# Kernel optimization log

Hardware: AMD Instinct MI355X
Metric: run time of the kernel (lower is better)

## Reference

```python
import jax, jax.numpy as jnp
from jax import lax
import numpy as np

B, L, D_MODEL = 2, 2048, 1024
D_INNER, D_STATE, D_CONV, DT_RANK = 2048, 16, 4, 64


def setup_inputs() -> dict:
    key = jax.random.key(0)
    ks = jax.random.split(key, 10)
    s = 0.02  # weight scale to keep activations numerically sane
    return {
        "x": jax.random.normal(ks[0], (B, L, D_MODEL), jnp.float32),
        "W_in": jax.random.normal(ks[1], (D_MODEL, 2 * D_INNER), jnp.float32) * s,
        "conv_w": jax.random.normal(ks[2], (D_INNER, D_CONV), jnp.float32) * 0.2,
        "conv_b": jax.random.normal(ks[3], (D_INNER,), jnp.float32) * 0.1,
        "W_xproj": jax.random.normal(ks[4], (D_INNER, DT_RANK + 2 * D_STATE), jnp.float32) * s,
        "W_dt": jax.random.normal(ks[5], (DT_RANK, D_INNER), jnp.float32) * (DT_RANK ** -0.5),
        "b_dt": jax.random.normal(ks[6], (D_INNER,), jnp.float32) * 0.1,
        "A_log": jax.random.uniform(ks[7], (D_INNER, D_STATE), jnp.float32),
        "D_skip": jnp.ones((D_INNER,), jnp.float32),
        "W_out": jax.random.normal(ks[8], (D_INNER, D_MODEL), jnp.float32) * s,
    }


def _causal_depthwise_conv(xt, w, b):
    # xt: (B, L, d_inner), w: (d_inner, d_conv). Torch pads both sides by d_conv-1
    # then slices [:L] => causal left-pad of d_conv-1.
    xc = jnp.moveaxis(xt, 1, 2)  # (B, d_inner, L)
    out = lax.conv_general_dilated(
        xc, w[:, None, :], window_strides=(1,),
        padding=[(D_CONV - 1, 0)], feature_group_count=D_INNER)
    return jnp.moveaxis(out, 1, 2) + b  # (B, L, d_inner)


def _selective_scan(u, delta, A, Bm, Cm, D_skip):
    # u, delta: (B, L, d_inner); A: (d_inner, d_state); Bm, Cm: (B, L, d_state)
    deltaA = jnp.exp(delta[..., None] * A)                  # (B,L,di,ds)
    dBu = (delta * u)[..., None] * Bm[:, :, None, :]        # (B,L,di,ds)

    def step(h, inp):
        dA_t, dBu_t, C_t = inp                              # (B,di,ds),(B,di,ds),(B,ds)
        h = dA_t * h + dBu_t
        y = jnp.einsum('bds,bs->bd', h, C_t)
        return h, y

    h0 = jnp.zeros((u.shape[0], D_INNER, D_STATE), u.dtype)
    xs = (jnp.moveaxis(deltaA, 1, 0), jnp.moveaxis(dBu, 1, 0), jnp.moveaxis(Cm, 1, 0))
    _, ys = lax.scan(step, h0, xs)                          # ys: (L,B,di)
    return jnp.moveaxis(ys, 0, 1) + u * D_skip


def reference(x, W_in, conv_w, conv_b, W_xproj, W_dt, b_dt, A_log, D_skip, W_out):
    xz = x @ W_in                                           # (B,L,2*di)
    xin, z = jnp.split(xz, 2, axis=-1)
    xc = jax.nn.silu(_causal_depthwise_conv(xin, conv_w, conv_b))
    dbc = xc @ W_xproj                                      # (B,L,dt_rank+2*ds)
    dt_lo = dbc[..., :DT_RANK]
    Bm = dbc[..., DT_RANK:DT_RANK + D_STATE]
    Cm = dbc[..., DT_RANK + D_STATE:]
    delta = jax.nn.softplus(dt_lo @ W_dt + b_dt)            # (B,L,di)
    A = -jnp.exp(A_log)
    y = _selective_scan(xc, delta, A, Bm, Cm, D_skip)
    return (y * jax.nn.silu(z)) @ W_out                     # (B,L,d_model)
```

## Files before the change

### kernel.cpp

```cpp
#include <hip/hip_runtime.h>
#include <math.h>

#define B_SZ 2
#define L_SZ 2048
#define DMODEL 1024
#define DINNER 2048
#define DSTATE 16
#define DCONV 4
#define DTRANK 64

#define CS 32
#define NCH (L_SZ / CS)

typedef float f32x4 __attribute__((ext_vector_type(4)));
typedef __bf16 bf16x8 __attribute__((ext_vector_type(8)));

__device__ __forceinline__ float silu_f(float x) {
    return x / (1.0f + __expf(-x));
}

__device__ __forceinline__ float softplus_f(float x) {
    return fmaxf(x, 0.0f) + __logf(1.0f + __expf(-fabsf(x)));
}

__device__ __forceinline__ unsigned short f2bf(float x) {
    unsigned int u = __float_as_uint(x);
    u = u + 0x7FFFu + ((u >> 16) & 1u);
    return (unsigned short)(u >> 16);
}

__device__ __forceinline__ float bf2f(unsigned short s) {
    return __uint_as_float(((unsigned int)s) << 16);
}

__device__ __forceinline__ void gload_lds16(const unsigned short* g, unsigned short* l) {
    __builtin_amdgcn_global_load_lds(
        (const __attribute__((address_space(1))) void*)g,
        (__attribute__((address_space(3))) void*)l, 16, 0, 0);
}

union Pack8 { unsigned short s[8]; uint4 v; };

__global__ __launch_bounds__(256) void transpose_cast(
    const float* __restrict__ W, unsigned short* __restrict__ WT, int R, int C)
{
    __shared__ float t[32][33];
    const int tx = threadIdx.x & 31;
    const int ty = threadIdx.x >> 5;
    const int r0 = blockIdx.y * 32;
    const int c0 = blockIdx.x * 32;
    #pragma unroll
    for (int i = 0; i < 4; i++)
        t[ty + i * 8][tx] = W[(r0 + ty + i * 8) * C + c0 + tx];
    __syncthreads();
    #pragma unroll
    for (int i = 0; i < 4; i++)
        WT[(c0 + ty + i * 8) * R + r0 + tx] = f2bf(t[tx][ty + i * 8]);
}

__global__ __launch_bounds__(256) void cast_bf16(
    const float* __restrict__ src, unsigned short* __restrict__ dst, int n8)
{
    int i = blockIdx.x * 256 + threadIdx.x;
    if (i >= n8) return;
    const float4 f0 = *(const float4*)(src + i * 8);
    const float4 f1 = *(const float4*)(src + i * 8 + 4);
    Pack8 p;
    p.s[0] = f2bf(f0.x); p.s[1] = f2bf(f0.y); p.s[2] = f2bf(f0.z); p.s[3] = f2bf(f0.w);
    p.s[4] = f2bf(f1.x); p.s[5] = f2bf(f1.y); p.s[6] = f2bf(f1.z); p.s[7] = f2bf(f1.w);
    *(uint4*)(dst + i * 8) = p.v;
}

template <int ACT, int OBF16>
__global__ __launch_bounds__(256) void gemm_bt_lds(
    const unsigned short* __restrict__ A, const unsigned short* __restrict__ BT,
    void* __restrict__ Cout, const float* __restrict__ bias,
    int M, int N, int K, int lda, int ldb, int ldc, int Kc)
{
    __shared__ unsigned short As[128 * 64];
    __shared__ unsigned short Bs[128 * 64];

    const int tid  = threadIdx.x;
    const int lane = tid & 63;
    const int wave = tid >> 6;
    const int wm   = wave >> 1;
    const int wn   = wave & 1;
    const int row0 = blockIdx.y * 128;
    const int col0 = blockIdx.x * 128;
    const int lq   = lane >> 4;
    const int lm   = lane & 15;
    const int kbeg = blockIdx.z * Kc;

    const int rloc = wave * 32 + (lane >> 3);
    const int sc   = (lane & 7) ^ ((lane >> 3) & 7);
    const unsigned short* gA = A + (size_t)(row0 + rloc) * lda + sc * 8;
    const unsigned short* gBp[4];
    #pragma unroll
    for (int is = 0; is < 4; is++) {
        int br = col0 + rloc + 8 * is;
        if (br > N - 1) br = N - 1;
        gBp[is] = BT + (size_t)br * ldb + sc * 8;
    }
    unsigned short* lA = As + wave * 2048;
    unsigned short* lB = Bs + wave * 2048;

    f32x4 acc[4][4];
    #pragma unroll
    for (int i = 0; i < 4; i++)
        #pragma unroll
        for (int j = 0; j < 4; j++)
            #pragma unroll
            for (int r = 0; r < 4; r++) acc[i][j][r] = 0.0f;

    for (int k0 = kbeg; k0 < kbeg + Kc; k0 += 64) {
        #pragma unroll
        for (int is = 0; is < 4; is++) {
            gload_lds16(gA + (size_t)(8 * is) * lda + k0, lA + is * 512);
            gload_lds16(gBp[is] + k0, lB + is * 512);
        }
        __syncthreads();

        #pragma unroll
        for (int ks = 0; ks < 2; ks++) {
            bf16x8 af[4], bfr[4];
            #pragma unroll
            for (int i = 0; i < 4; i++) {
                int row = wm * 64 + i * 16 + lm;
                af[i] = *(const bf16x8*)&As[row * 64 + (((ks * 4 + lq) ^ (row & 7)) * 8)];
            }
            #pragma unroll
            for (int j = 0; j < 4; j++) {
                int row = wn * 64 + j * 16 + lm;
                bfr[j] = *(const bf16x8*)&Bs[row * 64 + (((ks * 4 + lq) ^ (row & 7)) * 8)];
            }
            #pragma unroll
            for (int i = 0; i < 4; i++)
                #pragma unroll
                for (int j = 0; j < 4; j++)
                    acc[i][j] = __builtin_amdgcn_mfma_f32_16x16x32_bf16(
                        af[i], bfr[j], acc[i][j], 0, 0, 0);
        }
        __syncthreads();
    }

    #pragma unroll
    for (int i = 0; i < 4; i++) {
        #pragma unroll
        for (int r = 0; r < 4; r++) {
            int row = row0 + wm * 64 + i * 16 + lq * 4 + r;
            #pragma unroll
            for (int j = 0; j < 4; j++) {
                int col = col0 + wn * 64 + j * 16 + lm;
                if (col < N) {
                    float v = acc[i][j][r];
                    if (ACT == 1) v = softplus_f(v + bias[col]);
                    if (OBF16) {
                        unsigned short* Cz = (unsigned short*)Cout +
                            (size_t)blockIdx.z * (size_t)M * ldc;
                        Cz[(size_t)row * ldc + col] = f2bf(v);
                    } else {
                        float* Cz = (float*)Cout +
                            (size_t)blockIdx.z * (size_t)M * ldc;
                        Cz[(size_t)row * ldc + col] = v;
                    }
                }
            }
        }
    }
}

template <int OBF16>
__global__ __launch_bounds__(512, 2) void gemm_bt_256(
    const unsigned short* __restrict__ A, const unsigned short* __restrict__ BT,
    void* __restrict__ Cout, int M, int N, int K, int lda, int ldb, int ldc)
{
    __shared__ unsigned short sm[2][2][256 * 64];

    const int tid  = threadIdx.x;
    const int lane = tid & 63;
    const int wave = tid >> 6;
    const int wm   = wave >> 2;
    const int wn   = wave & 3;
    const int lq   = lane >> 4;
    const int lm   = lane & 15;

    const int cpx = gridDim.x >> 3;
    const int ti  = (blockIdx.x & 7) * cpx + (blockIdx.x >> 3);
    const int nbx = N >> 8;
    const int bx  = ti % nbx;
    const int by  = ti / nbx;
    const int row0 = by * 256;
    const int col0 = bx * 256;

    const int rA = tid >> 3;
    const int sc = (tid & 7) ^ (rA & 7);
    const unsigned short* gA = A + (size_t)(row0 + rA) * lda + sc * 8;
    const unsigned short* gB[4];
    #pragma unroll
    for (int a = 0; a < 4; a++) {
        int br = col0 + a * 64 + rA;
        if (br > N - 1) br = N - 1;
        gB[a] = BT + (size_t)br * ldb + sc * 8;
    }

    auto STAGE = [&](int bsel, int kk) {
        #pragma unroll
        for (int a = 0; a < 4; a++) {
            gload_lds16(gA + (size_t)(a * 64) * lda + kk,
                        &sm[bsel][0][a * 4096 + wave * 512]);
            gload_lds16(gB[a] + kk,
                        &sm[bsel][1][a * 4096 + wave * 512]);
        }
    };

    f32x4 acc[8][4];
    #pragma unroll
    for (int i = 0; i < 8; i++)
        #pragma unroll
        for (int j = 0; j < 4; j++)
            #pragma unroll
            for (int r = 0; r < 4; r++) acc[i][j][r] = 0.0f;

    const int NT = K >> 6;
    STAGE(0, 0);
    STAGE(1, 64);

    for (int t = 0; t < NT; ++t) {
        if (t < NT - 1) {
            asm volatile("s_waitcnt vmcnt(8)" ::: "memory");
        } else {
            asm volatile("s_waitcnt vmcnt(0)" ::: "memory");
        }
        __builtin_amdgcn_s_barrier();
        __builtin_amdgcn_sched_barrier(0);

        const int b = t & 1;
        #pragma unroll
        for (int ks = 0; ks < 2; ks++) {
            bf16x8 af[8], bq[4];
            #pragma unroll
            for (int i = 0; i < 8; i++) {
                int row = wm * 128 + i * 16 + lm;
                af[i] = *(const bf16x8*)&sm[b][0][row * 64 +
                            (((ks * 4 + lq) ^ (row & 7)) * 8)];
            }
            #pragma unroll
            for (int j = 0; j < 4; j++) {
                int row = wn * 64 + j * 16 + lm;
                bq[j] = *(const bf16x8*)&sm[b][1][row * 64 +
                            (((ks * 4 + lq) ^ (row & 7)) * 8)];
            }
            #pragma unroll
            for (int i = 0; i < 8; i++)
                #pragma unroll
                for (int j = 0; j < 4; j++)
                    acc[i][j] = __builtin_amdgcn_mfma_f32_16x16x32_bf16(
                        af[i], bq[j], acc[i][j], 0, 0, 0);
        }

        asm volatile("s_waitcnt lgkmcnt(0)" ::: "memory");
        __builtin_amdgcn_sched_barrier(0);
        __builtin_amdgcn_s_barrier();
        __builtin_amdgcn_sched_barrier(0);
        if (t + 2 < NT) STAGE(b, (t + 2) * 64);
    }

    #pragma unroll
    for (int i = 0; i < 8; i++) {
        #pragma unroll
        for (int r = 0; r < 4; r++) {
            int row = row0 + wm * 128 + i * 16 + lq * 4 + r;
            #pragma unroll
            for (int j = 0; j < 4; j++) {
                int col = col0 + wn * 64 + j * 16 + lm;
                if (col < N) {
                    float v = acc[i][j][r];
                    if (OBF16)
                        ((unsigned short*)Cout)[(size_t)row * ldc + col] = f2bf(v);
                    else
                        ((float*)Cout)[(size_t)row * ldc + col] = v;
                }
            }
        }
    }
}

__global__ __launch_bounds__(256) void reduce_splitk(
    const float* __restrict__ part, float* __restrict__ C,
    unsigned short* __restrict__ dtlo16, int n, int nsplit)
{
    int i = blockIdx.x * 256 + threadIdx.x;
    if (i >= n) return;
    float s = 0.0f;
    for (int z = 0; z < nsplit; z++) s += part[(size_t)z * n + i];
    C[i] = s;
    int row = i / 96;
    int col = i - row * 96;
    if (col < DTRANK) dtlo16[row * DTRANK + col] = f2bf(s);
}

__global__ __launch_bounds__(256) void conv_silu_v2(
    const unsigned short* __restrict__ xz16, const float* __restrict__ conv_w,
    const float* __restrict__ conv_b, unsigned short* __restrict__ xc16)
{
    const int tid = threadIdx.x;
    const int d   = blockIdx.x * 256 + tid;
    const int l0  = blockIdx.y * 32;
    const int b   = blockIdx.z;
    const float4 w  = *(const float4*)(conv_w + d * 4);
    const float bias = conv_b[d];
    const int t0 = b * L_SZ + l0;
    const unsigned short* src = xz16 + (size_t)t0 * 4096 + d;

    float r0, r1, r2;
    if (l0 == 0) {
        r0 = r1 = r2 = 0.0f;
    } else {
        r0 = bf2f(src[-3 * 4096]);
        r1 = bf2f(src[-2 * 4096]);
        r2 = bf2f(src[-1 * 4096]);
    }
    #pragma unroll 4
    for (int l = 0; l < 32; l++) {
        float r3 = bf2f(src[(size_t)l * 4096]);
        float acc = bias + r0 * w.x + r1 * w.y + r2 * w.z + r3 * w.w;
        xc16[(size_t)(t0 + l) * DINNER + d] = f2bf(silu_f(acc));
        r0 = r1; r1 = r2; r2 = r3;
    }
}

__global__ __launch_bounds__(256) void scan_pass1(
    const unsigned short* __restrict__ xc16, const float* __restrict__ delta,
    const float* __restrict__ dbc, const float* __restrict__ A_log,
    float* __restrict__ P, float* __restrict__ E)
{
    __shared__ float Bs[CS * DSTATE];
    const int tid = threadIdx.x;
    const int db  = blockIdx.x & 7;
    const int c   = (blockIdx.x >> 3) & (NCH - 1);
    const int b   = blockIdx.x >> 9;
    const int d   = db * 256 + tid;
    const int t0  = b * L_SZ + c * CS;

    for (int idx = tid; idx < CS * DSTATE; idx += 256) {
        int step = idx >> 4, i = idx & 15;
        Bs[idx] = dbc[(t0 + step) * 96 + DTRANK + i];
    }

    float A[DSTATE], Er[DSTATE];
    #pragma unroll
    for (int s = 0; s < DSTATE; s++) {
        A[s]  = -__expf(A_log[d * DSTATE + s]);
        Er[s] = 0.0f;
    }
    float sd = 0.0f;
    __syncthreads();

    for (int l = 0; l < CS; l++) {
        const int t = t0 + l;
        float dv = delta[t * DINNER + d];
        float uv = bf2f(xc16[(size_t)t * DINNER + d]);
        float du = dv * uv;
        sd += dv;
        #pragma unroll
        for (int s = 0; s < DSTATE; s++) {
            float dA = __expf(dv * A[s]);
            Er[s] = dA * Er[s] + du * Bs[l * DSTATE + s];
        }
    }

    const long long o = ((long long)((b * NCH + c) * DINNER) + d) * DSTATE;
    #pragma unroll
    for (int s = 0; s < DSTATE; s++) {
        P[o + s] = __expf(A[s] * sd);
        E[o + s] = Er[s];
    }
}

__global__ __launch_bounds__(256) void scan_pass2(
    const float* __restrict__ P, float* __restrict__ E)
{
    const int gid  = blockIdx.x * 256 + threadIdx.x;
    const int b    = gid >> 15;
    const int rest = gid & 32767;
    float h = 0.0f;
    for (int c = 0; c < NCH; c++) {
        const long long idx = (long long)(b * NCH + c) * (DINNER * DSTATE) + rest;
        float p = P[idx];
        float e = E[idx];
        E[idx] = h;
        h = p * h + e;
    }
}

__global__ __launch_bounds__(256) void scan_pass3(
    const unsigned short* __restrict__ xc16, const float* __restrict__ delta,
    const float* __restrict__ dbc, const float* __restrict__ A_log,
    const float* __restrict__ D_skip, const float* __restrict__ Hin,
    const unsigned short* __restrict__ xz16, unsigned short* __restrict__ y16)
{
    __shared__ float BCs[CS * 2 * DSTATE];
    const int tid = threadIdx.x;
    const int db  = blockIdx.x & 7;
    const int c   = (blockIdx.x >> 3) & (NCH - 1);
    const int b   = blockIdx.x >> 9;
    const int d   = db * 256 + tid;
    const int t0  = b * L_SZ + c * CS;

    for (int idx = tid; idx < CS * 2 * DSTATE; idx += 256) {
        int step = idx >> 5, i = idx & 31;
        BCs[idx] = dbc[(t0 + step) * 96 + DTRANK + i];
    }

    float A[DSTATE], h[DSTATE];
    const long long o = ((long long)((b * NCH + c) * DINNER) + d) * DSTATE;
    #pragma unroll
    for (int s = 0; s < DSTATE; s++) {
        A[s] = -__expf(A_log[d * DSTATE + s]);
        h[s] = Hin[o + s];
    }
    const float Dv = D_skip[d];
    __syncthreads();

    for (int l = 0; l < CS; l++) {
        const int t = t0 + l;
        float dv = delta[t * DINNER + d];
        float uv = bf2f(xc16[(size_t)t * DINNER + d]);
        float du = dv * uv;
        float yv = 0.0f;
        #pragma unroll
        for (int s = 0; s < DSTATE; s++) {
            float dA = __expf(dv * A[s]);
            h[s] = dA * h[s] + du * BCs[l * 32 + s];
            yv  += h[s] * BCs[l * 32 + DSTATE + s];
        }
        float z = bf2f(xz16[(size_t)t * 4096 + DINNER + d]);
        y16[t * DINNER + d] = f2bf((uv * Dv + yv) * silu_f(z));
    }
}

extern "C" void kernel_launch(void* const* d_in, const int* in_sizes, int n_in,
                              void* d_out, int out_size, void* d_ws, size_t ws_size,
                              hipStream_t stream) {
    const float* x       = (const float*)d_in[0];
    const float* W_in    = (const float*)d_in[1];
    const float* conv_w  = (const float*)d_in[2];
    const float* conv_b  = (const float*)d_in[3];
    const float* W_xproj = (const float*)d_in[4];
    const float* W_dt    = (const float*)d_in[5];
    const float* b_dt    = (const float*)d_in[6];
    const float* A_log   = (const float*)d_in[7];
    const float* D_skip  = (const float*)d_in[8];
    const float* W_out   = (const float*)d_in[9];
    float* out = (float*)d_out;

    float* ws = (float*)d_ws;
    unsigned short* xz16   = (unsigned short*)ws;
    unsigned short* xc16   = (unsigned short*)(ws +  8388608);
    float* dbc             = ws + 12582912;
    unsigned short* dtlo16 = (unsigned short*)(ws + 12976128);
    float* delta           = ws + 13107200;
    float* Ebuf            = ws + 21495808;
    float* Pbuf            = ws + 25690112;
    float* parts           = Pbuf;
    unsigned short* yb16   = (unsigned short*)(ws + 29884416);
    unsigned short* x16    = yb16;
    unsigned short* W_inT    = (unsigned short*)(ws + 31981568);
    unsigned short* W_xprojT = (unsigned short*)(ws + 34078720);
    unsigned short* W_dtT    = (unsigned short*)(ws + 34177024);
    unsigned short* W_outT   = (unsigned short*)(ws + 34242560);

    const int MT = 4096;

    transpose_cast<<<dim3(128, 32), 256, 0, stream>>>(W_in,    W_inT,    1024, 4096);
    transpose_cast<<<dim3(  3, 64), 256, 0, stream>>>(W_xproj, W_xprojT, 2048,   96);
    transpose_cast<<<dim3( 64,  2), 256, 0, stream>>>(W_dt,    W_dtT,      64, 2048);
    transpose_cast<<<dim3( 32, 64), 256, 0, stream>>>(W_out,   W_outT,   2048, 1024);
    cast_bf16<<<dim3(2048), 256, 0, stream>>>(x, x16, 524288);

    gemm_bt_256<1><<<dim3(256), 512, 0, stream>>>(
        x16, W_inT, xz16, MT, 4096, 1024, 1024, 1024, 4096);

    conv_silu_v2<<<dim3(8, 64, 2), 256, 0, stream>>>(xz16, conv_w, conv_b, xc16);

    gemm_bt_lds<0, 0><<<dim3(1, 32, 8), 256, 0, stream>>>(
        xc16, W_xprojT, parts, nullptr, MT, 96, 2048, 2048, 2048, 96, 256);
    reduce_splitk<<<dim3(1536), 256, 0, stream>>>(parts, dbc, dtlo16, MT * 96, 8);

    gemm_bt_lds<1, 0><<<dim3(16, 32), 256, 0, stream>>>(
        dtlo16, W_dtT, delta, b_dt, MT, 2048, 64, 64, 64, 2048, 64);

    scan_pass1<<<dim3(1024), 256, 0, stream>>>(xc16, delta, dbc, A_log, Pbuf, Ebuf);
    scan_pass2<<<dim3(256), 256, 0, stream>>>(Pbuf, Ebuf);
    scan_pass3<<<dim3(1024), 256, 0, stream>>>(xc16, delta, dbc, A_log, D_skip,
                                               Ebuf, xz16, yb16);

    gemm_bt_lds<0, 0><<<dim3(8, 32), 256, 0, stream>>>(
        yb16, W_outT, out, nullptr, MT, 1024, 2048, 2048, 2048, 1024, 2048);
}
```

Measured before the change: 319.3 us.

## Interleave GEMM loads with MFMA phases, split-K output GEMM, prefetch scan inputs

Rewrites the 256x256 GEMM into an 8-phase schedule. Global-to-LDS loads for the next two K tiles are spread across four MFMA sub-phases, with s_setprio raised around the MFMA blocks. The output projection now runs on this kernel with a 4-way split-K plus a vectorized reduction kernel, replacing the 128x? LDS GEMM. Both scan passes software-prefetch delta, u and z four steps ahead and read B/C from LDS as float4. Together these aim to hide memory latency and raise occupancy for the output GEMM. In exchange they add more barriers per tile, extra partial-sum traffic, and reuse of the delta buffer as scratch space.

```diff
diff --git a/kernel.cpp b/kernel.cpp
--- a/kernel.cpp
+++ b/kernel.cpp
@@ -170,11 +170,11 @@
 }
 
 template <int OBF16>
-__global__ __launch_bounds__(512, 2) void gemm_bt_256(
+__global__ __launch_bounds__(512, 2) void gemm_8ph(
     const unsigned short* __restrict__ A, const unsigned short* __restrict__ BT,
-    void* __restrict__ Cout, int M, int N, int K, int lda, int ldb, int ldc)
-{
-    __shared__ unsigned short sm[2][2][256 * 64];
+    void* __restrict__ Cout, int M, int N, int lda, int ldb, int ldc, int Kc)
+{
+    __shared__ unsigned short sm[2][2][4][64 * 64];
 
     const int tid  = threadIdx.x;
     const int lane = tid & 63;
@@ -187,31 +187,24 @@
     const int cpx = gridDim.x >> 3;
     const int ti  = (blockIdx.x & 7) * cpx + (blockIdx.x >> 3);
     const int nbx = N >> 8;
-    const int bx  = ti % nbx;
-    const int by  = ti / nbx;
-    const int row0 = by * 256;
-    const int col0 = bx * 256;
-
-    const int rA = tid >> 3;
-    const int sc = (tid & 7) ^ (rA & 7);
-    const unsigned short* gA = A + (size_t)(row0 + rA) * lda + sc * 8;
+    const int row0 = (ti / nbx) * 256;
+    const int col0 = (ti % nbx) * 256;
+    const int kbeg = blockIdx.z * Kc;
+
+    const int r  = tid >> 3;
+    const int sc = (tid & 7) ^ (r & 7);
+    const unsigned short* gA = A + (size_t)(row0 + r) * lda + sc * 8 + kbeg;
     const unsigned short* gB[4];
     #pragma unroll
-    for (int a = 0; a < 4; a++) {
-        int br = col0 + a * 64 + rA;
+    for (int u = 0; u < 4; u++) {
+        int br = col0 + u * 64 + r;
         if (br > N - 1) br = N - 1;
-        gB[a] = BT + (size_t)br * ldb + sc * 8;
-    }
-
-    auto STAGE = [&](int bsel, int kk) {
-        #pragma unroll
-        for (int a = 0; a < 4; a++) {
-            gload_lds16(gA + (size_t)(a * 64) * lda + kk,
-                        &sm[bsel][0][a * 4096 + wave * 512]);
-            gload_lds16(gB[a] + kk,
-                        &sm[bsel][1][a * 4096 + wave * 512]);
-        }
-    };
+        gB[u] = BT + (size_t)br * ldb + sc * 8 + kbeg;
+    }
+
+    #define STA(bsel, u, kk) gload_lds16(gA + (size_t)((u) * 64) * lda + (kk), \
+                                         &sm[bsel][0][u][wave * 512])
+    #define STB(bsel, u, kk) gload_lds16(gB[u] + (kk), &sm[bsel][1][u][wave * 512])
 
     f32x4 acc[8][4];
     #pragma unroll
@@ -219,66 +212,89 @@
         #pragma unroll
         for (int j = 0; j < 4; j++)
             #pragma unroll
-            for (int r = 0; r < 4; r++) acc[i][j][r] = 0.0f;
-
-    const int NT = K >> 6;
-    STAGE(0, 0);
-    STAGE(1, 64);
+            for (int rr = 0; rr < 4; rr++) acc[i][j][rr] = 0.0f;
+
+    const int NT = Kc >> 6;
+    STB(0, 0, 0); STB(0, 1, 0); STA(0, 0, 0); STA(0, 2, 0);
+    STA(0, 1, 0); STA(0, 3, 0); STB(0, 2, 0); STB(0, 3, 0);
+    if (NT > 1) { STB(1, 0, 64); STB(1, 1, 64); STA(1, 0, 64); STA(1, 2, 64); }
+
+    bf16x8 bq[4][2];
 
     for (int t = 0; t < NT; ++t) {
-        if (t < NT - 1) {
-            asm volatile("s_waitcnt vmcnt(8)" ::: "memory");
-        } else {
-            asm volatile("s_waitcnt vmcnt(0)" ::: "memory");
-        }
+        const int b   = t & 1;
+        const int kk1 = (t + 1) * 64;
+        const int kk2 = (t + 2) * 64;
+
+        if (t == NT - 1) asm volatile("s_waitcnt vmcnt(0)" ::: "memory");
+        else             asm volatile("s_waitcnt vmcnt(4)" ::: "memory");
         __builtin_amdgcn_s_barrier();
         __builtin_amdgcn_sched_barrier(0);
 
-        const int b = t & 1;
-        #pragma unroll
-        for (int ks = 0; ks < 2; ks++) {
-            bf16x8 af[8], bq[4];
-            #pragma unroll
-            for (int i = 0; i < 8; i++) {
-                int row = wm * 128 + i * 16 + lm;
-                af[i] = *(const bf16x8*)&sm[b][0][row * 64 +
-                            (((ks * 4 + lq) ^ (row & 7)) * 8)];
-            }
-            #pragma unroll
-            for (int j = 0; j < 4; j++) {
-                int row = wn * 64 + j * 16 + lm;
-                bq[j] = *(const bf16x8*)&sm[b][1][row * 64 +
-                            (((ks * 4 + lq) ^ (row & 7)) * 8)];
-            }
-            #pragma unroll
-            for (int i = 0; i < 8; i++)
+        #pragma unroll
+        for (int q = 0; q < 4; ++q) {
+            bf16x8 af2[2][2];
+            #pragma unroll
+            for (int ii = 0; ii < 2; ii++) {
+                int br = wm * 128 + (2 * q + ii) * 16 + lm;
                 #pragma unroll
-                for (int j = 0; j < 4; j++)
-                    acc[i][j] = __builtin_amdgcn_mfma_f32_16x16x32_bf16(
-                        af[i], bq[j], acc[i][j], 0, 0, 0);
-        }
-
-        asm volatile("s_waitcnt lgkmcnt(0)" ::: "memory");
-        __builtin_amdgcn_sched_barrier(0);
-        __builtin_amdgcn_s_barrier();
-        __builtin_amdgcn_sched_barrier(0);
-        if (t + 2 < NT) STAGE(b, (t + 2) * 64);
-    }
-
+                for (int ks = 0; ks < 2; ks++)
+                    af2[ii][ks] = *(const bf16x8*)&sm[b][0][br >> 6]
+                        [(br & 63) * 64 + (((ks * 4 + lq) ^ (br & 7)) * 8)];
+            }
+            if (q == 0) {
+                #pragma unroll
+                for (int j = 0; j < 4; j++) {
+                    int br = wn * 64 + j * 16 + lm;
+                    #pragma unroll
+                    for (int ks = 0; ks < 2; ks++)
+                        bq[j][ks] = *(const bf16x8*)&sm[b][1][br >> 6]
+                            [(br & 63) * 64 + (((ks * 4 + lq) ^ (br & 7)) * 8)];
+                }
+            }
+            if (q == 0 && t + 1 < NT) { STA(b ^ 1, 1, kk1); STA(b ^ 1, 3, kk1); }
+            if (q == 1 && t + 1 < NT) { STB(b ^ 1, 2, kk1); STB(b ^ 1, 3, kk1); }
+            if (q == 2 && t + 2 < NT) { STB(b, 0, kk2); STB(b, 1, kk2); }
+            if (q == 3 && t + 2 < NT) { STA(b, 0, kk2); STA(b, 2, kk2); }
+
+            asm volatile("s_waitcnt lgkmcnt(0)" ::: "memory");
+            __builtin_amdgcn_sched_barrier(0);
+            __builtin_amdgcn_s_setprio(1);
+            #pragma unroll
+            for (int ii = 0; ii < 2; ii++)
+                #pragma unroll
+                for (int j = 0; j < 4; j++) {
+                    acc[2 * q + ii][j] = __builtin_amdgcn_mfma_f32_16x16x32_bf16(
+                        af2[ii][0], bq[j][0], acc[2 * q + ii][j], 0, 0, 0);
+                    acc[2 * q + ii][j] = __builtin_amdgcn_mfma_f32_16x16x32_bf16(
+                        af2[ii][1], bq[j][1], acc[2 * q + ii][j], 0, 0, 0);
+                }
+            __builtin_amdgcn_s_setprio(0);
+            __builtin_amdgcn_sched_barrier(0);
+            if (q < 3) {
+                __builtin_amdgcn_s_barrier();
+                __builtin_amdgcn_sched_barrier(0);
+            }
+        }
+    }
+    #undef STA
+    #undef STB
+
+    const size_t zoff = (size_t)blockIdx.z * (size_t)M * ldc;
     #pragma unroll
     for (int i = 0; i < 8; i++) {
         #pragma unroll
-        for (int r = 0; r < 4; r++) {
-            int row = row0 + wm * 128 + i * 16 + lq * 4 + r;
+        for (int rr = 0; rr < 4; rr++) {
+            int row = row0 + wm * 128 + i * 16 + lq * 4 + rr;
             #pragma unroll
             for (int j = 0; j < 4; j++) {
                 int col = col0 + wn * 64 + j * 16 + lm;
                 if (col < N) {
-                    float v = acc[i][j][r];
+                    float v = acc[i][j][rr];
                     if (OBF16)
                         ((unsigned short*)Cout)[(size_t)row * ldc + col] = f2bf(v);
                     else
-                        ((float*)Cout)[(size_t)row * ldc + col] = v;
+                        ((float*)Cout)[zoff + (size_t)row * ldc + col] = v;
                 }
             }
         }
@@ -299,6 +315,19 @@
     if (col < DTRANK) dtlo16[row * DTRANK + col] = f2bf(s);
 }
 
+__global__ __launch_bounds__(256) void reduce4(
+    const float* __restrict__ part, float* __restrict__ out, int n4)
+{
+    int i = blockIdx.x * 256 + threadIdx.x;
+    if (i >= n4) return;
+    const f32x4* p = (const f32x4*)part;
+    f32x4 s = p[i];
+    s += p[i + n4];
+    s += p[i + 2 * n4];
+    s += p[i + 3 * n4];
+    ((f32x4*)out)[i] = s;
+}
+
 __global__ __launch_bounds__(256) void conv_silu_v2(
     const unsigned short* __restrict__ xz16, const float* __restrict__ conv_w,
     const float* __restrict__ conv_b, unsigned short* __restrict__ xc16)
@@ -354,19 +383,45 @@
         Er[s] = 0.0f;
     }
     float sd = 0.0f;
+
+    const float* dp = delta + (size_t)t0 * DINNER + d;
+    const unsigned short* up = xc16 + (size_t)t0 * DINNER + d;
+
+    float dv[4], uv[4];
+    #pragma unroll
+    for (int q = 0; q < 4; q++) {
+        dv[q] = dp[(size_t)q * DINNER];
+        uv[q] = bf2f(up[(size_t)q * DINNER]);
+    }
     __syncthreads();
 
-    for (int l = 0; l < CS; l++) {
-        const int t = t0 + l;
-        float dv = delta[t * DINNER + d];
-        float uv = bf2f(xc16[(size_t)t * DINNER + d]);
-        float du = dv * uv;
-        sd += dv;
-        #pragma unroll
-        for (int s = 0; s < DSTATE; s++) {
-            float dA = __expf(dv * A[s]);
-            Er[s] = dA * Er[s] + du * Bs[l * DSTATE + s];
-        }
+    for (int lo = 0; lo < CS; lo += 4) {
+        float nd[4], nu[4];
+        if (lo + 4 < CS) {
+            #pragma unroll
+            for (int q = 0; q < 4; q++) {
+                nd[q] = dp[(size_t)(lo + 4 + q) * DINNER];
+                nu[q] = bf2f(up[(size_t)(lo + 4 + q) * DINNER]);
+            }
+        }
+        #pragma unroll
+        for (int q = 0; q < 4; q++) {
+            const float dvq = dv[q];
+            const float du  = dvq * uv[q];
+            sd += dvq;
+            const f32x4* Bv = (const f32x4*)&Bs[(lo + q) * DSTATE];
+            #pragma unroll
+            for (int s4 = 0; s4 < 4; s4++) {
+                f32x4 bb = Bv[s4];
+                #pragma unroll
+                for (int k = 0; k < 4; k++) {
+                    int s = s4 * 4 + k;
+                    Er[s] = __expf(dvq * A[s]) * Er[s] + du * bb[k];
+                }
+            }
+        }
+        #pragma unroll
+        for (int q = 0; q < 4; q++) { dv[q] = nd[q]; uv[q] = nu[q]; }
     }
 
     const long long o = ((long long)((b * NCH + c) * DINNER) + d) * DSTATE;
@@ -420,22 +475,54 @@
         h[s] = Hin[o + s];
     }
     const float Dv = D_skip[d];
+
+    const float* dp = delta + (size_t)t0 * DINNER + d;
+    const unsigned short* up = xc16 + (size_t)t0 * DINNER + d;
+    const unsigned short* zp = xz16 + (size_t)t0 * 4096 + DINNER + d;
+    unsigned short* yp = y16 + (size_t)t0 * DINNER + d;
+
+    float dv[4], uv[4], zv[4];
+    #pragma unroll
+    for (int q = 0; q < 4; q++) {
+        dv[q] = dp[(size_t)q * DINNER];
+        uv[q] = bf2f(up[(size_t)q * DINNER]);
+        zv[q] = bf2f(zp[(size_t)q * 4096]);
+    }
     __syncthreads();
 
-    for (int l = 0; l < CS; l++) {
-        const int t = t0 + l;
-        float dv = delta[t * DINNER + d];
-        float uv = bf2f(xc16[(size_t)t * DINNER + d]);
-        float du = dv * uv;
-        float yv = 0.0f;
-        #pragma unroll
-        for (int s = 0; s < DSTATE; s++) {
-            float dA = __expf(dv * A[s]);
-            h[s] = dA * h[s] + du * BCs[l * 32 + s];
-            yv  += h[s] * BCs[l * 32 + DSTATE + s];
-        }
-        float z = bf2f(xz16[(size_t)t * 4096 + DINNER + d]);
-        y16[t * DINNER + d] = f2bf((uv * Dv + yv) * silu_f(z));
+    for (int lo = 0; lo < CS; lo += 4) {
+        float nd[4], nu[4], nz[4];
+        if (lo + 4 < CS) {
+            #pragma unroll
+            for (int q = 0; q < 4; q++) {
+                nd[q] = dp[(size_t)(lo + 4 + q) * DINNER];
+                nu[q] = bf2f(up[(size_t)(lo + 4 + q) * DINNER]);
+                nz[q] = bf2f(zp[(size_t)(lo + 4 + q) * 4096]);
+            }
+        }
+        #pragma unroll
+        for (int q = 0; q < 4; q++) {
+            const float dvq = dv[q];
+            const float uvq = uv[q];
+            const float du  = dvq * uvq;
+            const f32x4* Bv = (const f32x4*)&BCs[(lo + q) * 32];
+            float yv = 0.0f;
+            #pragma unroll
+            for (int s4 = 0; s4 < 4; s4++) {
+                f32x4 bb = Bv[s4];
+                f32x4 cc = Bv[4 + s4];
+                #pragma unroll
+                for (int k = 0; k < 4; k++) {
+                    int s = s4 * 4 + k;
+                    float dA = __expf(dvq * A[s]);
+                    h[s] = dA * h[s] + du * bb[k];
+                    yv  += h[s] * cc[k];
+                }
+            }
+            yp[(size_t)(lo + q) * DINNER] = f2bf((uvq * Dv + yv) * silu_f(zv[q]));
+        }
+        #pragma unroll
+        for (int q = 0; q < 4; q++) { dv[q] = nd[q]; uv[q] = nu[q]; zv[q] = nz[q]; }
     }
 }
 
@@ -463,6 +550,7 @@
     float* Ebuf            = ws + 21495808;
     float* Pbuf            = ws + 25690112;
     float* parts           = Pbuf;
+    float* parts6          = delta;
     unsigned short* yb16   = (unsigned short*)(ws + 29884416);
     unsigned short* x16    = yb16;
     unsigned short* W_inT    = (unsigned short*)(ws + 31981568);
@@ -478,8 +566,8 @@
     transpose_cast<<<dim3( 32, 64), 256, 0, stream>>>(W_out,   W_outT,   2048, 1024);
     cast_bf16<<<dim3(2048), 256, 0, stream>>>(x, x16, 524288);
 
-    gemm_bt_256<1><<<dim3(256), 512, 0, stream>>>(
-        x16, W_inT, xz16, MT, 4096, 1024, 1024, 1024, 4096);
+    gemm_8ph<1><<<dim3(256), 512, 0, stream>>>(
+        x16, W_inT, xz16, MT, 4096, 1024, 1024, 4096, 1024);
 
     conv_silu_v2<<<dim3(8, 64, 2), 256, 0, stream>>>(xz16, conv_w, conv_b, xc16);
 
@@ -495,6 +583,7 @@
     scan_pass3<<<dim3(1024), 256, 0, stream>>>(xc16, delta, dbc, A_log, D_skip,
                                                Ebuf, xz16, yb16);
 
-    gemm_bt_lds<0, 0><<<dim3(8, 32), 256, 0, stream>>>(
-        yb16, W_outT, out, nullptr, MT, 1024, 2048, 2048, 2048, 1024, 2048);
-}
+    gemm_8ph<0><<<dim3(64, 1, 4), 512, 0, stream>>>(
+        yb16, W_outT, parts6, MT, 1024, 2048, 2048, 1024, 512);
+    reduce4<<<dim3(4096), 256, 0, stream>>>(parts6, out, MT * 1024 / 4);
+}
```

After: 310.9 us. 2.6% less time.
